# Performance work log

Hardware: AMD Instinct MI355X
Metric: run time of the kernel (lower is better)

## Reference

```python
import jax, jax.numpy as jnp
import numpy as np

N, T, H, F, NZ, G = 768, 8, 128, 128, 64, 64
D = H + F + NZ  # DecoderFC input dim = 320


def _init(key, shape, scale=0.05):
    return jax.random.normal(key, shape, dtype=jnp.float32) * scale


def setup_inputs() -> dict:
    key = jax.random.key(0)
    ks = jax.random.split(key, 16)
    return dict(
        obsv_4d=jax.random.normal(ks[0], (N, T, 4), jnp.float32),
        noise=jax.random.normal(ks[1], (N, NZ), jnp.float32),
        W_emb=_init(ks[2], (H, 4)), b_emb=jnp.zeros((H,), jnp.float32),
        W_ih=_init(ks[3], (4 * H, H)), W_hh=_init(ks[4], (4 * H, H)),
        b_ih=jnp.zeros((4 * H,), jnp.float32), b_hh=jnp.zeros((4 * H,), jnp.float32),
        Wf1=_init(ks[5], (32, 3)), bf1=jnp.zeros((32,), jnp.float32),
        Wf2=_init(ks[6], (64, 32)), bf2=jnp.zeros((64,), jnp.float32),
        Wf3=_init(ks[7], (F, 64)), bf3=jnp.zeros((F,), jnp.float32),
        Wa=_init(ks[8], (F, H)), ba=jnp.zeros((F,), jnp.float32),
        Wd1=_init(ks[9], (D, D)), bd1=jnp.zeros((D,), jnp.float32),
        Wd2=_init(ks[10], (D // 2, D)), bd2=jnp.zeros((D // 2,), jnp.float32),
        Wd3=_init(ks[11], (D // 4, D // 2)), bd3=jnp.zeros((D // 4,), jnp.float32),
        Wd4=_init(ks[12], (2, D // 4)), bd4=jnp.zeros((2,), jnp.float32),
        n_next=12, group_size=G,
    )


def _lstm_cell(h, c, x, W_ih, W_hh, b_ih, b_hh):
    # PyTorch gate order: i, f, g, o
    z = x @ W_ih.T + h @ W_hh.T + b_ih + b_hh
    i, f, g, o = jnp.split(z, 4, axis=-1)
    c = jax.nn.sigmoid(f) * c + jax.nn.sigmoid(i) * jnp.tanh(g)
    h = jax.nn.sigmoid(o) * jnp.tanh(c)
    return h, c


def _social_features(x_last):
    # x_last: [N,4] = (px, py, vx, vy) at last observed step
    Dx = x_last[:, None, :] - x_last[None, :, :]          # [N,N,4]
    Dp, Dv = Dx[..., :2], Dx[..., 2:]
    l2 = jnp.linalg.norm(Dp, axis=2)                      # pairwise distance
    v = jnp.broadcast_to(x_last[:, None, 2:], Dp.shape)   # velocity of agent i
    cos = jnp.sum(Dp * v, -1) / (jnp.linalg.norm(Dp, axis=2) * jnp.linalg.norm(v, axis=2) + 1e-6)
    ttca = -jnp.sum(Dp * Dv, -1) / (jnp.sum(Dv * Dv, -1) + 1e-6)
    dca = jnp.linalg.norm(Dp + ttca[..., None] * Dv, axis=2)
    return jnp.stack([l2, cos, dca], axis=2)              # [N,N,3]


def _attention(f, h, Wa, ba, group_size):
    # Block-diagonal social attention pooling over equal-size sub-batches.
    n = h.shape[0]
    B = n // group_size
    Wh = h @ Wa.T + ba                                    # [N,F]
    fg = f.reshape(B, group_size, B, group_size, -1)
    fg = fg[jnp.arange(B), :, jnp.arange(B)]              # [B,G,G,F] diag blocks
    Whg = Wh.reshape(B, group_size, -1)
    hg = h.reshape(B, group_size, -1)
    sigma = jnp.einsum('bijf,bjf->bij', fg, Whg)          # [B,G,G]
    eye = jnp.eye(group_size, dtype=bool)
    sigma = jnp.where(eye[None], -1000.0, sigma)          # mask self, as in torch code
    attn = jax.nn.softmax(sigma, axis=2)
    S = jnp.einsum('bij,bjh->bih', attn, hg)              # [B,G,H]
    return S.reshape(n, -1)


def reference(obsv_4d, noise, W_emb, b_emb, W_ih, W_hh, b_ih, b_hh,
              Wf1, bf1, Wf2, bf2, Wf3, bf3, Wa, ba,
              Wd1, bd1, Wd2, bd2, Wd3, bd3, Wd4, bd4, n_next, group_size):
    n = obsv_4d.shape[0]
    hdim = W_hh.shape[1]
    # ---- encoder LSTM over observed trajectory ----
    x = obsv_4d @ W_emb.T + b_emb                         # [N,T,H]

    def enc_step(carry, xt):
        h, c = carry
        h, c = _lstm_cell(h, c, xt, W_ih, W_hh, b_ih, b_hh)
        return (h, c), None

    h0 = jnp.zeros((n, hdim), x.dtype)
    (h, c), _ = jax.lax.scan(enc_step, (h0, h0), jnp.swapaxes(x, 0, 1))
    # ---- social features + embedding + attention pooling ----
    feats = _social_features(obsv_4d[:, -1])              # [N,N,3]
    e = jax.nn.relu(feats @ Wf1.T + bf1)
    e = jax.nn.relu(e @ Wf2.T + bf2)
    f = e @ Wf3.T + bf3                                   # [N,N,F]
    weighted = _attention(f, h, Wa, ba, group_size)       # [N,H]
    lrelu = lambda u: jnp.where(u >= 0, u, 0.2 * u)

    def dec_fc(inp):
        u = lrelu(inp @ Wd1.T + bd1)
        u = lrelu(u @ Wd2.T + bd2)
        u = u @ Wd3.T + bd3
        return u @ Wd4.T + bd4

    def dec_step(carry, _):
        h, c, last = carry
        v = dec_fc(jnp.concatenate([h, weighted, noise], axis=1))  # [N,2]
        p = v + last[:, :2]
        new_last = jnp.concatenate([p, v], axis=1)                 # [N,4]
        xe = new_last @ W_emb.T + b_emb
        h, c = _lstm_cell(h, c, xe, W_ih, W_hh, b_ih, b_hh)
        return (h, c, new_last), new_last

    _, preds = jax.lax.scan(dec_step, (h, c, obsv_4d[:, -1]), None, length=n_next)
    return jnp.swapaxes(preds, 0, 1)                      # [N, n_next, 4]
```

## Files before the change

kernel.cpp:

```cpp
#include <hip/hip_runtime.h>
#include <math.h>

#define H_OFF    0
#define C_OFF    98304
#define G_OFF    196608
#define S0_OFF   245760
#define WTD_OFF  246528
#define TWA_OFF  475904
#define PKD1_OFF 492800
#define PKD2_OFF 544000
#define PKD3_OFF 569600
#define PKIH_OFF 576000
#define PKHH_OFF 608768

typedef short s8v __attribute__((ext_vector_type(8)));
typedef float f4v __attribute__((ext_vector_type(4)));

__device__ __forceinline__ float sigm(float x) { return 1.0f / (1.0f + __expf(-x)); }
__device__ __forceinline__ float ftanh(float x) { return 1.0f - 2.0f / (__expf(2.0f * x) + 1.0f); }
__device__ __forceinline__ float lrelu(float u) { return u >= 0.f ? u : 0.2f * u; }

__device__ __forceinline__ unsigned bf16rn(float f) {
  unsigned u = __float_as_uint(f);
  return (u + 0x7fffu + ((u >> 16) & 1u)) >> 16;
}
__device__ __forceinline__ unsigned pack2(float a, float b) {
  return bf16rn(a) | (bf16rn(b) << 16);
}
__device__ __forceinline__ int fidx(int a, int k) {
  int kt = k >> 5, kk = k & 31, half = kk >> 4, rem = kk & 15;
  return (kt * 64 + (rem >> 2) * 16 + a) * 8 + half * 4 + (rem & 3);
}

__device__ __forceinline__ void packB(const float* __restrict__ W, int K, int KT,
                                      unsigned* __restrict__ dst, int idx) {
  int t = idx >> 8, r = idx & 255, lane = r >> 2, d = r & 3;
  int nt = t / KT, kt = t % KT;
  int n = nt * 16 + (lane & 15), g = lane >> 4;
  int e0 = 2 * d, e1 = 2 * d + 1;
  int k0 = kt * 32 + ((e0 >> 2) << 4) + g * 4 + (e0 & 3);
  int k1 = kt * 32 + ((e1 >> 2) << 4) + g * 4 + (e1 & 3);
  dst[idx] = pack2(W[(size_t)n * K + k0], W[(size_t)n * K + k1]);
}

__global__ __launch_bounds__(256) void k_tr(
    const float* __restrict__ Wih, const float* __restrict__ Whh,
    const float* __restrict__ Wd1, const float* __restrict__ Wd2,
    const float* __restrict__ Wd3, const float* __restrict__ Wa,
    float* __restrict__ ws)
{
  const int idx = blockIdx.x * 256 + threadIdx.x;
  unsigned* wsu = (unsigned*)ws;
  if (idx < 16384) { int k = idx >> 7, r = idx & 127; ws[TWA_OFF + idx] = Wa[(size_t)r * 128 + k]; }
  if (idx < 51200) packB(Wd1, 320, 10, wsu + PKD1_OFF, idx);
  if (idx < 25600) packB(Wd2, 320, 10, wsu + PKD2_OFF, idx);
  if (idx < 6400)  packB(Wd3, 160, 5,  wsu + PKD3_OFF, idx);
  if (idx < 32768) {
    packB(Wih, 128, 4, wsu + PKIH_OFF, idx);
    packB(Whh, 128, 4, wsu + PKHH_OFF, idx);
  }
}

#define ZQUAD(Q, ZN, XEBUF, HBUF)                                                 \
    f4v ZN = {0.f, 0.f, 0.f, 0.f};                                               \
    {                                                                             \
      const int nt = wid + 8 * (Q);                                               \
      s8v Bv[4];                                                                  \
      _Pragma("unroll")                                                           \
      for (int kt = 0; kt < 4; ++kt)                                              \
        Bv[kt] = *(const s8v*)(pkih + ((size_t)(nt * 4 + kt) * 64 + lane) * 4);   \
      _Pragma("unroll")                                                           \
      for (int kt = 0; kt < 4; ++kt)                                              \
        ZN = __builtin_amdgcn_mfma_f32_16x16x32_bf16(                             \
            *(const s8v*)&XEBUF[(kt * 64 + lane) * 8], Bv[kt], ZN, 0, 0, 0);      \
      _Pragma("unroll")                                                           \
      for (int kt = 0; kt < 4; ++kt)                                              \
        Bv[kt] = *(const s8v*)(pkhh + ((size_t)(nt * 4 + kt) * 64 + lane) * 4);   \
      _Pragma("unroll")                                                           \
      for (int kt = 0; kt < 4; ++kt)                                              \
        ZN = __builtin_amdgcn_mfma_f32_16x16x32_bf16(                             \
            *(const s8v*)&HBUF[(kt * 64 + lane) * 8], Bv[kt], ZN, 0, 0, 0);       \
    }                                                                             \
    __builtin_amdgcn_sched_barrier(0);

__global__ __launch_bounds__(512) void k_enc(
    const float* __restrict__ obsv, const float* __restrict__ Wemb,
    const float* __restrict__ bemb, const float* __restrict__ bih,
    const float* __restrict__ bhh, float* __restrict__ ws)
{
  __shared__ __align__(16) unsigned short hF0[4 * 64 * 8];
  __shared__ __align__(16) unsigned short hF1[4 * 64 * 8];
  __shared__ __align__(16) unsigned short xeF[4 * 64 * 8];
  __shared__ float WembS[512], bembS[128];
  __shared__ float obS[16][32];

  const int tid = threadIdx.x;
  const int wid = tid >> 6, lane = tid & 63;
  const int n0 = blockIdx.x * 16;
  const int la = lane & 15, lg = lane >> 4;
  const int abase = lg * 4;

  const unsigned* pkih = (const unsigned*)(ws) + PKIH_OFF;
  const unsigned* pkhh = (const unsigned*)(ws) + PKHH_OFF;

  WembS[tid] = Wemb[tid];
  if (tid < 128) bembS[tid] = bemb[tid];
  {
    int a = tid >> 5, td = tid & 31;
    obS[a][td] = obsv[(size_t)(n0 + a) * 32 + td];
  }
  for (int e = tid; e < 2048; e += 512) hF0[e] = 0;

  f4v cReg = {0.f, 0.f, 0.f, 0.f};
  float bzR[4];
#pragma unroll
  for (int t = 0; t < 4; ++t) { int n = (wid + 8 * t) * 16 + la; bzR[t] = bih[n] + bhh[n]; }
  __syncthreads();

  for (int step = 0; step < 8; ++step) {
    unsigned short* hCur = (step & 1) ? hF1 : hF0;
    unsigned short* hNxt = (step & 1) ? hF0 : hF1;

    {
      int a = tid & 15, jj = tid >> 4;
      float l0 = obS[a][step * 4 + 0], l1 = obS[a][step * 4 + 1];
      float l2v = obS[a][step * 4 + 2], l3 = obS[a][step * 4 + 3];
#pragma unroll
      for (int p = 0; p < 4; ++p) {
        int j = jj + 32 * p;
        float4 w = *(const float4*)&WembS[j * 4];
        float xv = bembS[j] + l0 * w.x + l1 * w.y + l2v * w.z + l3 * w.w;
        xeF[fidx(a, j)] = (unsigned short)bf16rn(xv);
      }
    }
    __syncthreads();
    {
      ZQUAD(0, z0, xeF, hCur)
      ZQUAD(1, z1, xeF, hCur)
      ZQUAD(2, z2, xeF, hCur)
      ZQUAD(3, z3, xeF, hCur)
      int j = wid * 16 + la;
#pragma unroll
      for (int r = 0; r < 4; ++r) {
        float ci = sigm(z1[r] + bzR[1]) * cReg[r]
                 + sigm(z0[r] + bzR[0]) * ftanh(z2[r] + bzR[2]);
        cReg[r] = ci;
        float hv = sigm(z3[r] + bzR[3]) * ftanh(ci);
        hNxt[fidx(abase + r, j)] = (unsigned short)bf16rn(hv);
        if (step == 7) {
          ws[H_OFF + (size_t)(n0 + abase + r) * 128 + j] = hv;
          ws[C_OFF + (size_t)(n0 + abase + r) * 128 + j] = ci;
        }
      }
    }
    __syncthreads();
  }
}

__global__ __launch_bounds__(128) void k_social(
    const float* __restrict__ ba, const float* __restrict__ Wf3,
    const float* __restrict__ bf3, float* __restrict__ ws)
{
  __shared__ float hsh[128];
  __shared__ float Wh[128];
  const int n = blockIdx.x, t = threadIdx.x;
  hsh[t] = ws[H_OFF + (size_t)n * 128 + t];
  __syncthreads();
  float acc = ba[t];
#pragma unroll 8
  for (int k = 0; k < 128; ++k) acc += ws[TWA_OFF + (size_t)k * 128 + t] * hsh[k];
  Wh[t] = acc;
  __syncthreads();
  if (t < 64) {
    float g = 0.f;
#pragma unroll 8
    for (int f = 0; f < 128; ++f) g += Wf3[(size_t)f * 64 + t] * Wh[f];
    ws[G_OFF + (size_t)n * 64 + t] = g;
  } else {
    int l = t - 64;
    float p = bf3[l] * Wh[l] + bf3[l + 64] * Wh[l + 64];
    for (int off = 32; off > 0; off >>= 1) p += __shfl_xor(p, off);
    if (l == 0) ws[S0_OFF + n] = p;
  }
}

__global__ __launch_bounds__(64) void k_attn(
    const float* __restrict__ obsv, const float* __restrict__ Wf1,
    const float* __restrict__ bf1, const float* __restrict__ Wf2,
    const float* __restrict__ bf2, float* __restrict__ ws)
{
  __shared__ float w1[96];
  __shared__ float b1[32];
  __shared__ float w2[2048];
  __shared__ float b2[64];
  __shared__ float attn_s[64];
  __shared__ float xi[4];

  const int i = blockIdx.x;
  const int b = i >> 6;
  const int lane = threadIdx.x;
  const int jn = (b << 6) + lane;

  for (int e = lane; e < 96; e += 64) w1[e] = Wf1[e];
  if (lane < 32) b1[lane] = bf1[lane];
  for (int e = lane; e < 2048; e += 64) w2[e] = Wf2[e];
  b2[lane] = bf2[lane];
  if (lane < 4) xi[lane] = obsv[((size_t)i * 8 + 7) * 4 + lane];
  __syncthreads();

  float4 xj = *(const float4*)&obsv[((size_t)jn * 8 + 7) * 4];
  float dpx = xi[0] - xj.x, dpy = xi[1] - xj.y;
  float vix = xi[2], viy = xi[3];
  float dvx = vix - xj.z, dvy = viy - xj.w;
  float l2 = sqrtf(dpx * dpx + dpy * dpy);
  float vnorm = sqrtf(vix * vix + viy * viy);
  float cosv = (dpx * vix + dpy * viy) / (l2 * vnorm + 1e-6f);
  float dv2 = dvx * dvx + dvy * dvy;
  float ttca = -(dpx * dvx + dpy * dvy) / (dv2 + 1e-6f);
  float cax = dpx + ttca * dvx, cay = dpy + ttca * dvy;
  float dca = sqrtf(cax * cax + cay * cay);

  float e1[32];
#pragma unroll
  for (int r = 0; r < 32; ++r)
    e1[r] = fmaxf(w1[r * 3 + 0] * l2 + w1[r * 3 + 1] * cosv + w1[r * 3 + 2] * dca + b1[r], 0.f);

  const float* gp = &ws[G_OFF + (size_t)jn * 64];
  float sig = ws[S0_OFF + jn];
  for (int r = 0; r < 64; ++r) {
    float a2 = b2[r];
#pragma unroll
    for (int k4 = 0; k4 < 8; ++k4) {
      float4 w = *(const float4*)&w2[r * 32 + k4 * 4];
      a2 += w.x * e1[k4 * 4 + 0] + w.y * e1[k4 * 4 + 1] + w.z * e1[k4 * 4 + 2] + w.w * e1[k4 * 4 + 3];
    }
    a2 = fmaxf(a2, 0.f);
    sig += a2 * gp[r];
  }
  if (lane == (i & 63)) sig = -1000.f;

  float m = sig;
  for (int off = 32; off > 0; off >>= 1) m = fmaxf(m, __shfl_xor(m, off));
  float ex = __expf(sig - m);
  float ssum = ex;
  for (int off = 32; off > 0; off >>= 1) ssum += __shfl_xor(ssum, off);
  attn_s[lane] = ex / ssum;
  __syncthreads();

  const float* hbase = &ws[H_OFF + (size_t)(b << 6) * 128];
  float s0a = 0.f, s1a = 0.f;
  for (int j = 0; j < 64; ++j) {
    float aj = attn_s[j];
    s0a += aj * hbase[(size_t)j * 128 + lane];
    s1a += aj * hbase[(size_t)j * 128 + 64 + lane];
  }
  ws[WTD_OFF + (size_t)i * 128 + lane] = s0a;
  ws[WTD_OFF + (size_t)i * 128 + 64 + lane] = s1a;
}

__global__ __launch_bounds__(512) void k_dec(
    const float* __restrict__ obsv, const float* __restrict__ noise,
    const float* __restrict__ Wemb, const float* __restrict__ bemb,
    const float* __restrict__ bd1, const float* __restrict__ bd2,
    const float* __restrict__ bd3, const float* __restrict__ bd4,
    const float* __restrict__ Wd4, const float* __restrict__ bih,
    const float* __restrict__ bhh,
    float* __restrict__ ws, float* __restrict__ out)
{
  __shared__ __align__(16) unsigned short hF0[4 * 64 * 8];
  __shared__ __align__(16) unsigned short hF1[4 * 64 * 8];
  __shared__ __align__(16) unsigned short swF[6 * 64 * 8];
  __shared__ __align__(16) unsigned short u1F[10 * 64 * 8];
  __shared__ __align__(16) unsigned short u2F[5 * 64 * 8];
  __shared__ __align__(16) unsigned short xeF[4 * 64 * 8];
  __shared__ float u3S[16 * 84];
  __shared__ float lastS[64];
  __shared__ float Wd4S[160], bd4S2[2];
  __shared__ float WembS[512], bembS[128];
  __shared__ float bd1S[320], bd2S[160], bd3S[80];

  const int tid = threadIdx.x;
  const int wid = tid >> 6, lane = tid & 63;
  const int n0 = blockIdx.x * 16;
  const int la = lane & 15, lg = lane >> 4;
  const int abase = lg * 4;

  const unsigned* pkd1 = (const unsigned*)(ws) + PKD1_OFF;
  const unsigned* pkd2 = (const unsigned*)(ws) + PKD2_OFF;
  const unsigned* pkd3 = (const unsigned*)(ws) + PKD3_OFF;
  const unsigned* pkih = (const unsigned*)(ws) + PKIH_OFF;
  const unsigned* pkhh = (const unsigned*)(ws) + PKHH_OFF;

  {
    int a = tid & 15, jj = tid >> 4;
#pragma unroll 4
    for (int p = 0; p < 4; ++p) {
      int j = jj + 32 * p;
      hF0[fidx(a, j)] = (unsigned short)bf16rn(ws[H_OFF + (size_t)(n0 + a) * 128 + j]);
      swF[fidx(a, j)] = (unsigned short)bf16rn(ws[WTD_OFF + (size_t)(n0 + a) * 128 + j]);
    }
#pragma unroll 2
    for (int p = 0; p < 2; ++p) {
      int j = jj + 32 * p;
      swF[fidx(a, 128 + j)] = (unsigned short)bf16rn(noise[(size_t)(n0 + a) * 64 + j]);
    }
  }
  if (tid < 64) lastS[tid] = obsv[((size_t)(n0 + (tid >> 2)) * 8 + 7) * 4 + (tid & 3)];
  if (tid < 160) Wd4S[tid] = Wd4[tid];
  if (tid < 2) bd4S2[tid] = bd4[tid];
  WembS[tid] = Wemb[tid];
  if (tid < 128) bembS[tid] = bemb[tid];
  if (tid < 320) bd1S[tid] = bd1[tid];
  if (tid < 160) bd2S[tid] = bd2[tid];
  if (tid < 80) bd3S[tid] = bd3[tid];

  f4v cReg;
  {
    int j = wid * 16 + la;
#pragma unroll
    for (int r = 0; r < 4; ++r)
      cReg[r] = ws[C_OFF + (size_t)(n0 + abase + r) * 128 + j];
  }
  float bzR[4];
#pragma unroll
  for (int t = 0; t < 4; ++t) { int n = (wid + 8 * t) * 16 + la; bzR[t] = bih[n] + bhh[n]; }
  __syncthreads();

  for (int s = 0; s < 12; ++s) {
    unsigned short* hCur = (s & 1) ? hF1 : hF0;
    unsigned short* hNxt = (s & 1) ? hF0 : hF1;

#define A320(kt) (*(const s8v*)((kt) < 4 ? &hCur[((kt) * 64 + lane) * 8] : &swF[(((kt) - 4) * 64 + lane) * 8]))

    for (int nt = wid; nt < 20; nt += 8) {
      s8v Bv[10];
#pragma unroll
      for (int kt = 0; kt < 10; ++kt)
        Bv[kt] = *(const s8v*)(pkd1 + ((size_t)(nt * 10 + kt) * 64 + lane) * 4);
      f4v acc = {0.f, 0.f, 0.f, 0.f};
#pragma unroll
      for (int kt = 0; kt < 10; ++kt)
        acc = __builtin_amdgcn_mfma_f32_16x16x32_bf16(A320(kt), Bv[kt], acc, 0, 0, 0);
      int n = nt * 16 + la;
      float bias = bd1S[n];
#pragma unroll
      for (int r = 0; r < 4; ++r)
        u1F[fidx(abase + r, n)] = (unsigned short)bf16rn(lrelu(acc[r] + bias));
    }
#undef A320
    __syncthreads();
    for (int nt = wid; nt < 10; nt += 8) {
      s8v Bv[10];
#pragma unroll
      for (int kt = 0; kt < 10; ++kt)
        Bv[kt] = *(const s8v*)(pkd2 + ((size_t)(nt * 10 + kt) * 64 + lane) * 4);
      f4v acc = {0.f, 0.f, 0.f, 0.f};
#pragma unroll
      for (int kt = 0; kt < 10; ++kt)
        acc = __builtin_amdgcn_mfma_f32_16x16x32_bf16(
            *(const s8v*)&u1F[(kt * 64 + lane) * 8], Bv[kt], acc, 0, 0, 0);
      int n = nt * 16 + la;
      float bias = bd2S[n];
#pragma unroll
      for (int r = 0; r < 4; ++r)
        u2F[fidx(abase + r, n)] = (unsigned short)bf16rn(lrelu(acc[r] + bias));
    }
    __syncthreads();
    if (wid < 5) {
      s8v Bv[5];
#pragma unroll
      for (int kt = 0; kt < 5; ++kt)
        Bv[kt] = *(const s8v*)(pkd3 + ((size_t)(wid * 5 + kt) * 64 + lane) * 4);
      f4v acc = {0.f, 0.f, 0.f, 0.f};
#pragma unroll
      for (int kt = 0; kt < 5; ++kt)
        acc = __builtin_amdgcn_mfma_f32_16x16x32_bf16(
            *(const s8v*)&u2F[(kt * 64 + lane) * 8], Bv[kt], acc, 0, 0, 0);
      int n = wid * 16 + la;
      float bias = bd3S[n];
#pragma unroll
      for (int r = 0; r < 4; ++r)
        u3S[(abase + r) * 84 + n] = acc[r] + bias;
    }
    __syncthreads();
    if (tid < 128) {
      int a = tid >> 3, r = (tid >> 2) & 1, q = tid & 3;
      float part = 0.f;
#pragma unroll
      for (int i = q * 20; i < q * 20 + 20; ++i)
        part += Wd4S[r * 80 + i] * u3S[a * 84 + i];
      part += __shfl_xor(part, 1);
      part += __shfl_xor(part, 2);
      if (q == 0) {
        float v = part + bd4S2[r];
        float p = v + lastS[a * 4 + r];
        lastS[a * 4 + r] = p;
        lastS[a * 4 + 2 + r] = v;
        out[(size_t)(n0 + a) * 48 + s * 4 + r] = p;
        out[(size_t)(n0 + a) * 48 + s * 4 + 2 + r] = v;
      }
    }
    __syncthreads();
    {
      int a = tid & 15, jj = tid >> 4;
      float l0 = lastS[a * 4 + 0], l1 = lastS[a * 4 + 1];
      float l2v = lastS[a * 4 + 2], l3 = lastS[a * 4 + 3];
#pragma unroll
      for (int p = 0; p < 4; ++p) {
        int j = jj + 32 * p;
        float4 w = *(const float4*)&WembS[j * 4];
        float xv = bembS[j] + l0 * w.x + l1 * w.y + l2v * w.z + l3 * w.w;
        xeF[fidx(a, j)] = (unsigned short)bf16rn(xv);
      }
    }
    __syncthreads();
    {
      ZQUAD(0, z0, xeF, hCur)
      ZQUAD(1, z1, xeF, hCur)
      ZQUAD(2, z2, xeF, hCur)
      ZQUAD(3, z3, xeF, hCur)
      int j = wid * 16 + la;
#pragma unroll
      for (int r = 0; r < 4; ++r) {
        float ci = sigm(z1[r] + bzR[1]) * cReg[r]
                 + sigm(z0[r] + bzR[0]) * ftanh(z2[r] + bzR[2]);
        cReg[r] = ci;
        float hv = sigm(z3[r] + bzR[3]) * ftanh(ci);
        hNxt[fidx(abase + r, j)] = (unsigned short)bf16rn(hv);
      }
    }
    __syncthreads();
  }
}

extern "C" void kernel_launch(void* const* d_in, const int* in_sizes, int n_in,
                              void* d_out, int out_size, void* d_ws, size_t ws_size,
                              hipStream_t stream)
{
  const float* obsv = (const float*)d_in[0];
  const float* noise = (const float*)d_in[1];
  const float* Wemb = (const float*)d_in[2];
  const float* bemb = (const float*)d_in[3];
  const float* Wih = (const float*)d_in[4];
  const float* Whh = (const float*)d_in[5];
  const float* bih = (const float*)d_in[6];
  const float* bhh = (const float*)d_in[7];
  const float* Wf1 = (const float*)d_in[8];
  const float* bf1 = (const float*)d_in[9];
  const float* Wf2 = (const float*)d_in[10];
  const float* bf2 = (const float*)d_in[11];
  const float* Wf3 = (const float*)d_in[12];
  const float* bf3 = (const float*)d_in[13];
  const float* Wa = (const float*)d_in[14];
  const float* ba = (const float*)d_in[15];
  const float* Wd1 = (const float*)d_in[16];
  const float* bd1 = (const float*)d_in[17];
  const float* Wd2 = (const float*)d_in[18];
  const float* bd2 = (const float*)d_in[19];
  const float* Wd3 = (const float*)d_in[20];
  const float* bd3 = (const float*)d_in[21];
  const float* Wd4 = (const float*)d_in[22];
  const float* bd4 = (const float*)d_in[23];
  float* ws = (float*)d_ws;
  float* out = (float*)d_out;

  k_tr<<<200, 256, 0, stream>>>(Wih, Whh, Wd1, Wd2, Wd3, Wa, ws);
  k_enc<<<48, 512, 0, stream>>>(obsv, Wemb, bemb, bih, bhh, ws);
  k_social<<<768, 128, 0, stream>>>(ba, Wf3, bf3, ws);
  k_attn<<<768, 64, 0, stream>>>(obsv, Wf1, bf1, Wf2, bf2, ws);
  k_dec<<<48, 512, 0, stream>>>(obsv, noise, Wemb, bemb, bd1, bd2, bd3, bd4, Wd4,
                                bih, bhh, ws, out);
}
```

Baseline: 163.6 us.

## Double decoder block threads and stage LSTM gates through shared memory

The decoder kernel now runs 1024 threads per block instead of 512. The LSTM gate GEMM is split across 16 waves, each writing gate pre-activations plus bias into a shared zS buffer. The cell state moves from registers into shared memory (cS), and a separate elementwise pass computes the new c and h. The encoder LSTM step is also reordered to compute one gate quad at a time, which lowers register pressure. The extra waves are meant to shorten each serial decoder step, at the cost of more LDS use and one extra barrier per step.

```diff
diff --git a/kernel.cpp b/kernel.cpp
--- a/kernel.cpp
+++ b/kernel.cpp
@@ -135,21 +135,34 @@
     }
     __syncthreads();
     {
-      ZQUAD(0, z0, xeF, hCur)
-      ZQUAD(1, z1, xeF, hCur)
-      ZQUAD(2, z2, xeF, hCur)
-      ZQUAD(3, z3, xeF, hCur)
-      int j = wid * 16 + la;
-#pragma unroll
-      for (int r = 0; r < 4; ++r) {
-        float ci = sigm(z1[r] + bzR[1]) * cReg[r]
-                 + sigm(z0[r] + bzR[0]) * ftanh(z2[r] + bzR[2]);
-        cReg[r] = ci;
-        float hv = sigm(z3[r] + bzR[3]) * ftanh(ci);
-        hNxt[fidx(abase + r, j)] = (unsigned short)bf16rn(hv);
-        if (step == 7) {
-          ws[H_OFF + (size_t)(n0 + abase + r) * 128 + j] = hv;
-          ws[C_OFF + (size_t)(n0 + abase + r) * 128 + j] = ci;
+      f4v tg;
+      {
+        ZQUAD(2, z2, xeF, hCur)
+#pragma unroll
+        for (int r = 0; r < 4; ++r) tg[r] = ftanh(z2[r] + bzR[2]);
+      }
+      f4v cip;
+      {
+        ZQUAD(0, z0, xeF, hCur)
+#pragma unroll
+        for (int r = 0; r < 4; ++r) cip[r] = sigm(z0[r] + bzR[0]) * tg[r];
+      }
+      {
+        ZQUAD(1, z1, xeF, hCur)
+#pragma unroll
+        for (int r = 0; r < 4; ++r) cReg[r] = sigm(z1[r] + bzR[1]) * cReg[r] + cip[r];
+      }
+      {
+        ZQUAD(3, z3, xeF, hCur)
+        int j = wid * 16 + la;
+#pragma unroll
+        for (int r = 0; r < 4; ++r) {
+          float hv = sigm(z3[r] + bzR[3]) * ftanh(cReg[r]);
+          hNxt[fidx(abase + r, j)] = (unsigned short)bf16rn(hv);
+          if (step == 7) {
+            ws[H_OFF + (size_t)(n0 + abase + r) * 128 + j] = hv;
+            ws[C_OFF + (size_t)(n0 + abase + r) * 128 + j] = cReg[r];
+          }
         }
       }
     }
@@ -258,7 +271,7 @@
   ws[WTD_OFF + (size_t)i * 128 + 64 + lane] = s1a;
 }
 
-__global__ __launch_bounds__(512) void k_dec(
+__global__ __launch_bounds__(1024) void k_dec(
     const float* __restrict__ obsv, const float* __restrict__ noise,
     const float* __restrict__ Wemb, const float* __restrict__ bemb,
     const float* __restrict__ bd1, const float* __restrict__ bd2,
@@ -273,10 +286,12 @@
   __shared__ __align__(16) unsigned short u1F[10 * 64 * 8];
   __shared__ __align__(16) unsigned short u2F[5 * 64 * 8];
   __shared__ __align__(16) unsigned short xeF[4 * 64 * 8];
+  __shared__ float zS[16 * 520];
+  __shared__ float cS[16 * 128];
   __shared__ float u3S[16 * 84];
   __shared__ float lastS[64];
   __shared__ float Wd4S[160], bd4S2[2];
-  __shared__ float WembS[512], bembS[128];
+  __shared__ float WembS[512], bembS[128], bzS[512];
   __shared__ float bd1S[320], bd2S[160], bd3S[80];
 
   const int tid = threadIdx.x;
@@ -293,37 +308,26 @@
 
   {
     int a = tid & 15, jj = tid >> 4;
-#pragma unroll 4
-    for (int p = 0; p < 4; ++p) {
-      int j = jj + 32 * p;
+#pragma unroll 2
+    for (int p = 0; p < 2; ++p) {
+      int j = jj + 64 * p;
       hF0[fidx(a, j)] = (unsigned short)bf16rn(ws[H_OFF + (size_t)(n0 + a) * 128 + j]);
       swF[fidx(a, j)] = (unsigned short)bf16rn(ws[WTD_OFF + (size_t)(n0 + a) * 128 + j]);
-    }
-#pragma unroll 2
-    for (int p = 0; p < 2; ++p) {
-      int j = jj + 32 * p;
+      cS[a * 128 + j] = ws[C_OFF + (size_t)(n0 + a) * 128 + j];
+    }
+    {
+      int j = jj;
       swF[fidx(a, 128 + j)] = (unsigned short)bf16rn(noise[(size_t)(n0 + a) * 64 + j]);
     }
   }
   if (tid < 64) lastS[tid] = obsv[((size_t)(n0 + (tid >> 2)) * 8 + 7) * 4 + (tid & 3)];
   if (tid < 160) Wd4S[tid] = Wd4[tid];
   if (tid < 2) bd4S2[tid] = bd4[tid];
-  WembS[tid] = Wemb[tid];
+  if (tid < 512) { WembS[tid] = Wemb[tid]; bzS[tid] = bih[tid] + bhh[tid]; }
   if (tid < 128) bembS[tid] = bemb[tid];
   if (tid < 320) bd1S[tid] = bd1[tid];
   if (tid < 160) bd2S[tid] = bd2[tid];
   if (tid < 80) bd3S[tid] = bd3[tid];
-
-  f4v cReg;
-  {
-    int j = wid * 16 + la;
-#pragma unroll
-    for (int r = 0; r < 4; ++r)
-      cReg[r] = ws[C_OFF + (size_t)(n0 + abase + r) * 128 + j];
-  }
-  float bzR[4];
-#pragma unroll
-  for (int t = 0; t < 4; ++t) { int n = (wid + 8 * t) * 16 + la; bzR[t] = bih[n] + bhh[n]; }
   __syncthreads();
 
   for (int s = 0; s < 12; ++s) {
@@ -332,7 +336,7 @@
 
 #define A320(kt) (*(const s8v*)((kt) < 4 ? &hCur[((kt) * 64 + lane) * 8] : &swF[(((kt) - 4) * 64 + lane) * 8]))
 
-    for (int nt = wid; nt < 20; nt += 8) {
+    for (int nt = wid; nt < 20; nt += 16) {
       s8v Bv[10];
 #pragma unroll
       for (int kt = 0; kt < 10; ++kt)
@@ -349,7 +353,8 @@
     }
 #undef A320
     __syncthreads();
-    for (int nt = wid; nt < 10; nt += 8) {
+    if (wid < 10) {
+      int nt = wid;
       s8v Bv[10];
 #pragma unroll
       for (int kt = 0; kt < 10; ++kt)
@@ -405,28 +410,48 @@
       int a = tid & 15, jj = tid >> 4;
       float l0 = lastS[a * 4 + 0], l1 = lastS[a * 4 + 1];
       float l2v = lastS[a * 4 + 2], l3 = lastS[a * 4 + 3];
-#pragma unroll
-      for (int p = 0; p < 4; ++p) {
-        int j = jj + 32 * p;
+#pragma unroll 2
+      for (int p = 0; p < 2; ++p) {
+        int j = jj + 64 * p;
         float4 w = *(const float4*)&WembS[j * 4];
         float xv = bembS[j] + l0 * w.x + l1 * w.y + l2v * w.z + l3 * w.w;
         xeF[fidx(a, j)] = (unsigned short)bf16rn(xv);
       }
     }
     __syncthreads();
+    for (int nt = wid; nt < 32; nt += 16) {
+      s8v Bv[8];
+#pragma unroll
+      for (int kt = 0; kt < 4; ++kt) {
+        Bv[kt]     = *(const s8v*)(pkih + ((size_t)(nt * 4 + kt) * 64 + lane) * 4);
+        Bv[4 + kt] = *(const s8v*)(pkhh + ((size_t)(nt * 4 + kt) * 64 + lane) * 4);
+      }
+      f4v acc = {0.f, 0.f, 0.f, 0.f};
+#pragma unroll
+      for (int kt = 0; kt < 4; ++kt)
+        acc = __builtin_amdgcn_mfma_f32_16x16x32_bf16(
+            *(const s8v*)&xeF[(kt * 64 + lane) * 8], Bv[kt], acc, 0, 0, 0);
+#pragma unroll
+      for (int kt = 0; kt < 4; ++kt)
+        acc = __builtin_amdgcn_mfma_f32_16x16x32_bf16(
+            *(const s8v*)&hCur[(kt * 64 + lane) * 8], Bv[4 + kt], acc, 0, 0, 0);
+      int n = nt * 16 + la;
+      float bz = bzS[n];
+#pragma unroll
+      for (int r = 0; r < 4; ++r)
+        zS[(abase + r) * 520 + n] = acc[r] + bz;
+    }
+    __syncthreads();
     {
-      ZQUAD(0, z0, xeF, hCur)
-      ZQUAD(1, z1, xeF, hCur)
-      ZQUAD(2, z2, xeF, hCur)
-      ZQUAD(3, z3, xeF, hCur)
-      int j = wid * 16 + la;
-#pragma unroll
-      for (int r = 0; r < 4; ++r) {
-        float ci = sigm(z1[r] + bzR[1]) * cReg[r]
-                 + sigm(z0[r] + bzR[0]) * ftanh(z2[r] + bzR[2]);
-        cReg[r] = ci;
-        float hv = sigm(z3[r] + bzR[3]) * ftanh(ci);
-        hNxt[fidx(abase + r, j)] = (unsigned short)bf16rn(hv);
+      int a = tid & 15, jj = tid >> 4;
+#pragma unroll 2
+      for (int p = 0; p < 2; ++p) {
+        int j = jj + 64 * p;
+        const float* zp = &zS[a * 520];
+        float ci = sigm(zp[128 + j]) * cS[a * 128 + j] + sigm(zp[j]) * ftanh(zp[256 + j]);
+        cS[a * 128 + j] = ci;
+        float hv = sigm(zp[384 + j]) * ftanh(ci);
+        hNxt[fidx(a, j)] = (unsigned short)bf16rn(hv);
       }
     }
     __syncthreads();
@@ -468,6 +493,6 @@
   k_enc<<<48, 512, 0, stream>>>(obsv, Wemb, bemb, bih, bhh, ws);
   k_social<<<768, 128, 0, stream>>>(ba, Wf3, bf3, ws);
   k_attn<<<768, 64, 0, stream>>>(obsv, Wf1, bf1, Wf2, bf2, ws);
-  k_dec<<<48, 512, 0, stream>>>(obsv, noise, Wemb, bemb, bd1, bd2, bd3, bd4, Wd4,
-                                bih, bhh, ws, out);
-}
+  k_dec<<<48, 1024, 0, stream>>>(obsv, noise, Wemb, bemb, bd1, bd2, bd3, bd4, Wd4,
+                                 bih, bhh, ws, out);
+}
```

New measurement: 184.0 us. +12.5%, slower.
